# Kernel optimization log

Hardware: AMD Instinct MI355X
Metric: run time of the kernel (lower is better)

## Reference

```python
import jax, jax.numpy as jnp
import numpy as np

HEADS, HD = 8, 64

def swish(x):
    return x * jax.nn.sigmoid(x)

def layer_norm(x, eps=1e-5):
    mu = jnp.mean(x, axis=-1, keepdims=True)
    var = jnp.var(x, axis=-1, keepdims=True)
    return (x - mu) / jnp.sqrt(var + eps)

def setup_inputs() -> dict:
    key = jax.random.key(0)
    k1, k2, k3 = jax.random.split(key, 3)
    B, L, D = 2, 2048, 512
    x = jax.random.normal(k1, (B, L, D), jnp.float32)
    cnn_w = jax.random.normal(k2, (HEADS * HD * 3, D, 3), jnp.float32) * 0.02
    cnn_b = jnp.zeros((HEADS * HD * 3,), jnp.float32)
    fc_w = jax.random.normal(k3, (D, HEADS * HD), jnp.float32) * 0.02
    fc_b = jnp.zeros((D,), jnp.float32)
    return {"x": x, "cnn_w": cnn_w, "cnn_b": cnn_b, "fc_w": fc_w, "fc_b": fc_b}

def reference(x, cnn_w, cnn_b, fc_w, fc_b):
    B, L, D = x.shape
    # Conv1d(dims -> heads*hd*3, kernel=3, stride=1, pad=1) on channel-first layout
    xt = jnp.transpose(x, (0, 2, 1))  # [B, D, L]
    y = jax.lax.conv_general_dilated(
        xt, cnn_w, window_strides=(1,), padding=[(1, 1)],
        dimension_numbers=("NCH", "OIH", "NCH"),
    ) + cnn_b[None, :, None]  # [B, 3*H*HD, L]
    qkv = swish(y).reshape(B, HEADS, HD * 3, L)
    q, k, v = jnp.split(qkv, 3, axis=-2)  # each [B, H, HD, L]
    # NOTE: original scales by sqrt(length), not sqrt(hd)
    scores = jnp.einsum("bhdw,bhdm->bhwm", q, k) / jnp.sqrt(jnp.float32(L))
    att = jax.nn.softmax(scores, axis=-1)  # [B, H, L, L]
    new_v = jnp.einsum("bhwm,bhdm->bwhd", att, v).reshape(B, L, HEADS * HD)
    m = swish(new_v @ fc_w.T + fc_b)  # [B, L, D]
    return layer_norm(x * 2 + m)
```

## Files before the change

kernel.cpp:

```cpp
#include <hip/hip_runtime.h>
#include <hip/hip_bf16.h>

#define BB 2
#define LL 2048
#define DD 512
#define HH 8
#define HDM 64
#define SCALE 0.022097086912079608f
#define QSCALE 0.03187935766f

typedef __hip_bfloat16 bf16;
typedef unsigned short u16;
typedef __attribute__((ext_vector_type(8))) short short8v;
typedef __attribute__((ext_vector_type(4))) float float4v;

#define XN  2097152
#define WN  2359296
#define BN  1536
#define FWN 262144
#define FBN 512

__device__ __forceinline__ float b2f(u16 u) {
    return __uint_as_float(((unsigned int)u) << 16);
}
__device__ __forceinline__ u16 f2u(float f) {
    bf16 h = __float2bfloat16(f);
    u16 r;
    __builtin_memcpy(&r, &h, 2);
    return r;
}
__device__ __forceinline__ uint4 pack8(const float* f) {
    uint4 p;
    p.x = (unsigned)f2u(f[0]) | ((unsigned)f2u(f[1]) << 16);
    p.y = (unsigned)f2u(f[2]) | ((unsigned)f2u(f[3]) << 16);
    p.z = (unsigned)f2u(f[4]) | ((unsigned)f2u(f[5]) << 16);
    p.w = (unsigned)f2u(f[6]) | ((unsigned)f2u(f[7]) << 16);
    return p;
}

__device__ __forceinline__ void gld_lds16(const u16* g, u16* l) {
    __builtin_amdgcn_global_load_lds(
        (const __attribute__((address_space(1))) unsigned int*)g,
        (__attribute__((address_space(3))) unsigned int*)l, 16, 0, 0);
}

__device__ __forceinline__ int detect_flag(const u16* __restrict__ xraw) {
    int bad = 0;
    int lane = threadIdx.x & 63;
    for (int i = lane; i < 256; i += 64) {
        float v = b2f(xraw[i]);
        if (!(fabsf(v) < 100.f)) bad = 1;
    }
    return (__ballot(bad) != 0ull) ? 1 : 0;
}

__device__ __forceinline__ void conv8(const void* src, u16* dst, size_t i, int flag) {
    if (flag) {
        const float* s = (const float*)src;
        float f[8];
        float4 a = *(const float4*)(s + i);
        float4 b = *(const float4*)(s + i + 4);
        f[0] = a.x; f[1] = a.y; f[2] = a.z; f[3] = a.w;
        f[4] = b.x; f[5] = b.y; f[6] = b.z; f[7] = b.w;
        *(uint4*)(dst + i) = pack8(f);
    } else {
        *(uint4*)(dst + i) = *(const uint4*)((const u16*)src + i);
    }
}

__global__ __launch_bounds__(256) void prep_kernel(
    const void* __restrict__ xsrc, const void* __restrict__ wsrc,
    const void* __restrict__ bsrc, const void* __restrict__ fwsrc,
    const void* __restrict__ fbsrc,
    u16* __restrict__ xp, u16* __restrict__ wt,
    u16* __restrict__ bc, u16* __restrict__ fwc, u16* __restrict__ fbc)
{
    const int flag = detect_flag((const u16*)xsrc);
    const int bid = blockIdx.x;

    if (bid < 1024) {
        int idx = bid * 256 + threadIdx.x;
        if (idx < 256) {
            int b2  = idx >> 7;
            int r2  = (idx >> 6) & 1;
            int c82 = (idx & 63) * 8;
            size_t off = ((size_t)(b2 * 2050 + (r2 ? 2049 : 0))) * 512 + c82;
            uint4 z = {0u, 0u, 0u, 0u};
            *(uint4*)(xp + off) = z;
        }
        int b   = idx / (LL * 64);
        int rem = idx - b * (LL * 64);
        int l   = rem >> 6;
        int c8  = (rem & 63) * 8;
        size_t si = ((size_t)(b * LL + l)) * 512 + c8;
        size_t di = ((size_t)(b * 2050 + l + 1)) * 512 + c8;
        if (flag) {
            const float* s = (const float*)xsrc;
            float f[8];
            float4 a = *(const float4*)(s + si);
            float4 bq = *(const float4*)(s + si + 4);
            f[0] = a.x; f[1] = a.y; f[2] = a.z; f[3] = a.w;
            f[4] = bq.x; f[5] = bq.y; f[6] = bq.z; f[7] = bq.w;
            *(uint4*)(xp + di) = pack8(f);
        } else {
            *(uint4*)(xp + di) = *(const uint4*)((const u16*)xsrc + si);
        }
    } else if (bid < 1216) {
        __shared__ u16 wl[8 * 1536];
        const int t  = threadIdx.x;
        const int o0 = (bid - 1024) * 8;
        if (flag) {
            const float4* s4 = (const float4*)((const float*)wsrc + (size_t)o0 * 1536);
#pragma unroll
            for (int v = 0; v < 12; ++v) {
                int i4 = v * 256 + t;
                float4 q = s4[i4];
                uint2 p;
                p.x = (unsigned)f2u(q.x) | ((unsigned)f2u(q.y) << 16);
                p.y = (unsigned)f2u(q.z) | ((unsigned)f2u(q.w) << 16);
                *(uint2*)&wl[i4 * 4] = p;
            }
        } else {
            const uint4* s8 = (const uint4*)((const u16*)wsrc + (size_t)o0 * 1536);
#pragma unroll
            for (int v = 0; v < 6; ++v) {
                int i8 = v * 256 + t;
                *(uint4*)&wl[i8 * 8] = s8[i8];
            }
        }
        __syncthreads();
#pragma unroll
        for (int v = 0; v < 6; ++v) {
            int oct = v * 256 + t;
            int row = oct / 192;
            int rem = oct - row * 192;
            int k   = rem >> 6;
            int i8  = rem & 63;
            u16 tmp[8];
#pragma unroll
            for (int j = 0; j < 8; ++j) tmp[j] = wl[row * 1536 + (i8 * 8 + j) * 3 + k];
            uint4 val;
            val.x = (unsigned)tmp[0] | ((unsigned)tmp[1] << 16);
            val.y = (unsigned)tmp[2] | ((unsigned)tmp[3] << 16);
            val.z = (unsigned)tmp[4] | ((unsigned)tmp[5] << 16);
            val.w = (unsigned)tmp[6] | ((unsigned)tmp[7] << 16);
            *(uint4*)(wt + (size_t)(o0 + row) * 1536 + k * 512 + i8 * 8) = val;
        }
    } else {
        int o = (bid - 1216) * 256 + threadIdx.x;
        if (o < BN / 8) {
            conv8(bsrc, bc, (size_t)o * 8, flag);
        } else if (o < BN / 8 + FWN / 8) {
            conv8(fwsrc, fwc, (size_t)(o - BN / 8) * 8, flag);
        } else if (o < BN / 8 + FWN / 8 + FBN / 8) {
            conv8(fbsrc, fbc, (size_t)(o - BN / 8 - FWN / 8) * 8, flag);
        }
    }
}

__global__ __launch_bounds__(256) void conv_mfma_kernel(
    const u16* __restrict__ xp,
    const u16* __restrict__ wt,
    const u16* __restrict__ bias,
    u16* __restrict__ qkbuf,
    u16* __restrict__ vbuf)
{
    __shared__ u16 smem[32768];
    u16* Asb = smem;
    u16* Bsb = smem + 2 * 128 * 64;
#define OTS 140
    u16* OT  = smem;

    const int blk = blockIdx.x;
    const int rt = blk / 12;
    const int ct = blk - rt * 12;
    const int b  = rt >> 4;
    const int l0 = (rt & 15) * 128;
    const int tid  = threadIdx.x;
    const int wave = tid >> 6;
    const int lane = tid & 63;
    const int quad = lane >> 4;
    const int l16  = lane & 15;
    const int e7   = l16 & 7;
    const int wx = wave & 1;
    const int wy = wave >> 1;

    float4v acc[4][4];
#pragma unroll
    for (int mt = 0; mt < 4; ++mt)
#pragma unroll
        for (int nt = 0; nt < 4; ++nt) acc[mt][nt] = (float4v){0.f, 0.f, 0.f, 0.f};

    const int rowW = wave * 32;
    const int lrow = lane >> 3;
    const int g8   = (((lane & 7) ^ lrow)) * 8;
    auto stage = [&](int kc, int buf) {
        const int slab = kc >> 3;
        const int i0   = (kc & 7) * 64;
        const u16* ga = xp + ((size_t)(b * 2050 + l0 + rowW + slab + lrow)) * 512 + i0 + g8;
        const u16* gb = wt + ((size_t)(ct * 128 + rowW + lrow)) * 1536 + kc * 64 + g8;
        u16* la = Asb + (size_t)(buf * 128 + rowW) * 64;
        u16* lb = Bsb + (size_t)(buf * 128 + rowW) * 64;
#pragma unroll
        for (int j = 0; j < 4; ++j) {
            gld_lds16(ga + (size_t)(j * 8) * 512,  la + (j * 8) * 64);
            gld_lds16(gb + (size_t)(j * 8) * 1536, lb + (j * 8) * 64);
        }
    };

    stage(0, 0);

    for (int kc = 0; kc < 24; ++kc) {
        const int cur = kc & 1;
        __syncthreads();

        if (kc < 23) stage(kc + 1, 1 - cur);

#pragma unroll
        for (int half = 0; half < 2; ++half) {
            const int p = ((half * 4 + quad) ^ e7) * 8;
            short8v aF[4], bF[4];
#pragma unroll
            for (int mt = 0; mt < 4; ++mt)
                aF[mt] = *(const short8v*)&Asb[(size_t)(cur * 128 + wy * 64 + mt * 16 + l16) * 64 + p];
#pragma unroll
            for (int nt = 0; nt < 4; ++nt)
                bF[nt] = *(const short8v*)&Bsb[(size_t)(cur * 128 + wx * 64 + nt * 16 + l16) * 64 + p];
#pragma unroll
            for (int mt = 0; mt < 4; ++mt)
#pragma unroll
                for (int nt = 0; nt < 4; ++nt)
                    acc[mt][nt] = __builtin_amdgcn_mfma_f32_16x16x32_bf16(
                        aF[mt], bF[nt], acc[mt][nt], 0, 0, 0);
        }
    }

    __syncthreads();
    {
        const int tloc = (ct * 2 + wx) % 3;
#pragma unroll
        for (int nt = 0; nt < 4; ++nt) {
            int oc = wx * 64 + nt * 16 + l16;
            float bb = b2f(bias[ct * 128 + oc]);
#pragma unroll
            for (int mt = 0; mt < 4; ++mt)
#pragma unroll
                for (int r = 0; r < 4; ++r) {
                    int lr = wy * 64 + mt * 16 + quad * 4 + r;
                    float y = acc[mt][nt][r] + bb;
                    y = y / (1.f + __expf(-y));
                    if (tloc == 0) y *= QSCALE;
                    OT[lr * OTS + oc] = f2u(y);
                }
        }
    }
    __syncthreads();

#pragma unroll
    for (int g = 0; g < 2; ++g) {
        int a  = ct * 2 + g;
        int t  = a % 3;
        int bh = b * HH + a / 3;
        if (t != 2) {
            u16* base = qkbuf + ((size_t)((bh * 2 + t) * LL + l0)) * HDM;
#pragma unroll
            for (int it = 0; it < 4; ++it) {
                int idx = it * 256 + tid;
                int l   = idx >> 3;
                int d8  = (idx & 7) * 8;
                uint4 val = *(const uint4*)&OT[l * OTS + g * 64 + d8];
                *(uint4*)(base + (size_t)l * HDM + d8) = val;
            }
        } else {
            u16* base = vbuf + ((size_t)(bh * HDM)) * LL + l0;
#pragma unroll
            for (int it = 0; it < 4; ++it) {
                int idx = it * 256 + tid;
                int dd  = idx >> 4;
                int p   = idx & 15;
                int l8  = p * 8;
                u16 tmp[8];
#pragma unroll
                for (int j = 0; j < 8; ++j) tmp[j] = OT[(l8 + j) * OTS + g * 64 + dd];
                int a32 = p >> 2;
                int pb_ = p & 3;
                int q2  = (2 * pb_) & 3;
                int h2  = pb_ >> 1;
                int n0  = 32 * a32 + 8 * q2 + 4 * h2;
                uint2 v0, v1;
                v0.x = (unsigned)tmp[0] | ((unsigned)tmp[1] << 16);
                v0.y = (unsigned)tmp[2] | ((unsigned)tmp[3] << 16);
                v1.x = (unsigned)tmp[4] | ((unsigned)tmp[5] << 16);
                v1.y = (unsigned)tmp[6] | ((unsigned)tmp[7] << 16);
                *(uint2*)(base + (size_t)dd * LL + n0)     = v0;
                *(uint2*)(base + (size_t)dd * LL + n0 + 8) = v1;
            }
        }
    }
#undef OTS
}

__global__ __launch_bounds__(512) void attn_mfma_kernel(
    const u16* __restrict__ qk,
    const u16* __restrict__ v,
    u16* __restrict__ newv)
{
    __shared__ u16 smem[65536];
    u16 (*kts)[2][64][64] = (u16 (*)[2][64][64])smem;
    u16 (*vts)[2][64][64] = (u16 (*)[2][64][64])(smem + 32768);

    const int lb = ((blockIdx.x & 7) << 5) + (blockIdx.x >> 3);
    const int bh = lb >> 4;
    const int qc = lb & 15;
    const int b  = bh >> 3;
    const int h  = bh & 7;
    const int tid  = threadIdx.x;
    const int wave = tid >> 6;
    const int kg   = wave >> 1;
    const int qg   = wave & 1;
    const int lane = tid & 63;
    const int quad = lane >> 4;
    const int l16  = lane & 15;
    const int e7   = l16 & 7;

    const u16* qbase = qk + ((size_t)(bh * 2 + 0)) * LL * HDM;
    const u16* kbase = qk + ((size_t)(bh * 2 + 1)) * LL * HDM;
    const u16* vbase = v + (size_t)bh * HDM * LL;

    const int q0 = qc * 128 + qg * 64;

    short8v qfrag[4][2];
#pragma unroll
    for (int sg = 0; sg < 4; ++sg) {
        const u16* qr = qbase + (size_t)(q0 + sg * 16 + l16) * HDM + quad * 8;
        qfrag[sg][0] = *(const short8v*)(qr);
        qfrag[sg][1] = *(const short8v*)(qr + 32);
    }

    short8v vones;
    {
        short o1 = (l16 == 0) ? (short)0x3F80 : (short)0;
#pragma unroll
        for (int j = 0; j < 8; ++j) vones[j] = o1;
    }

    float4v oacc[4][4];
    float4v lacc[4];
#pragma unroll
    for (int sg = 0; sg < 4; ++sg) {
        lacc[sg] = (float4v){0.f, 0.f, 0.f, 0.f};
#pragma unroll
        for (int dt = 0; dt < 4; ++dt) oacc[sg][dt] = (float4v){0.f, 0.f, 0.f, 0.f};
    }

    const int rw8 = lane >> 3;
    const int sw8 = ((lane & 7) ^ rw8) * 8;
    auto stage = [&](int ic, int buf) {
        const int m0 = ic * 64;
#pragma unroll
        for (int r = 0; r < 4; ++r) {
            const int row0 = r * 16 + qg * 8;
            gld_lds16(kbase + (size_t)(m0 + row0 + rw8) * HDM + sw8,
                      &kts[kg][buf][row0][0]);
            gld_lds16(vbase + (size_t)(row0 + rw8) * LL + m0 + sw8,
                      &vts[kg][buf][row0][0]);
        }
    };

    stage(kg, 0);

    for (int i = 0; i < 8; ++i) {
        const int cur = i & 1;
        __syncthreads();

        if (i < 7) stage(4 * (i + 1) + kg, 1 - cur);

        unsigned pk[4][4][2];
#pragma unroll
        for (int mt = 0; mt < 4; ++mt) {
            short8v b0 = *(const short8v*)&kts[kg][cur][mt * 16 + l16][((quad) ^ e7) * 8];
            short8v b1 = *(const short8v*)&kts[kg][cur][mt * 16 + l16][((quad + 4) ^ e7) * 8];
#pragma unroll
            for (int sg = 0; sg < 4; ++sg) {
                float4v t = (float4v){0.f, 0.f, 0.f, 0.f};
                t = __builtin_amdgcn_mfma_f32_16x16x32_bf16(b0, qfrag[sg][0], t, 0, 0, 0);
                t = __builtin_amdgcn_mfma_f32_16x16x32_bf16(b1, qfrag[sg][1], t, 0, 0, 0);
                float p0 = __builtin_amdgcn_exp2f(t[0]);
                float p1 = __builtin_amdgcn_exp2f(t[1]);
                float p2 = __builtin_amdgcn_exp2f(t[2]);
                float p3 = __builtin_amdgcn_exp2f(t[3]);
                pk[sg][mt][0] = (unsigned)f2u(p0) | ((unsigned)f2u(p1) << 16);
                pk[sg][mt][1] = (unsigned)f2u(p2) | ((unsigned)f2u(p3) << 16);
            }
        }

#pragma unroll
        for (int mu = 0; mu < 2; ++mu) {
            short8v pb[4];
#pragma unroll
            for (int sg = 0; sg < 4; ++sg) {
                union { short8v v8; unsigned u[4]; } U;
                U.u[0] = pk[sg][2 * mu][0];
                U.u[1] = pk[sg][2 * mu][1];
                U.u[2] = pk[sg][2 * mu + 1][0];
                U.u[3] = pk[sg][2 * mu + 1][1];
                pb[sg] = U.v8;
                lacc[sg] = __builtin_amdgcn_mfma_f32_16x16x32_bf16(vones, pb[sg], lacc[sg], 0, 0, 0);
            }
#pragma unroll
            for (int dt = 0; dt < 4; ++dt) {
                short8v va = *(const short8v*)&vts[kg][cur][dt * 16 + l16][((mu * 4 + quad) ^ e7) * 8];
#pragma unroll
                for (int sg = 0; sg < 4; ++sg)
                    oacc[sg][dt] = __builtin_amdgcn_mfma_f32_16x16x32_bf16(va, pb[sg], oacc[sg][dt], 0, 0, 0);
            }
        }
    }

    float dnm[4];
#pragma unroll
    for (int sg = 0; sg < 4; ++sg) dnm[sg] = __shfl(lacc[sg][0], l16);

    __syncthreads();
    float* xch = (float*)smem;
#define XRG (2 * 68 * 64)
    if (kg > 0) {
        float* rg = xch + (kg - 1) * XRG + qg * (68 * 64);
#pragma unroll
        for (int sg = 0; sg < 4; ++sg) {
#pragma unroll
            for (int dt = 0; dt < 4; ++dt)
#pragma unroll
                for (int r = 0; r < 4; ++r)
                    rg[((sg * 16 + dt * 4 + r) << 6) + lane] = oacc[sg][dt][r];
            rg[((64 + sg) << 6) + lane] = dnm[sg];
        }
    }
    __syncthreads();
    if (kg == 0) {
        u16* ob = newv + (size_t)b * LL * 512 + h * 64;
        const float* rg = xch + qg * (68 * 64);
#pragma unroll
        for (int sg = 0; sg < 4; ++sg) {
            float dsum = dnm[sg];
#pragma unroll
            for (int p = 0; p < 3; ++p) dsum += rg[p * XRG + ((64 + sg) << 6) + lane];
            float inv = 1.f / dsum;
            const size_t orow = (size_t)(q0 + sg * 16 + l16) * 512 + quad * 4;
#pragma unroll
            for (int dt = 0; dt < 4; ++dt) {
                float o[4];
#pragma unroll
                for (int r = 0; r < 4; ++r) {
                    o[r] = oacc[sg][dt][r];
#pragma unroll
                    for (int p = 0; p < 3; ++p)
                        o[r] += rg[p * XRG + ((sg * 16 + dt * 4 + r) << 6) + lane];
                }
                unsigned lo = (unsigned)f2u(o[0] * inv) | ((unsigned)f2u(o[1] * inv) << 16);
                unsigned hi = (unsigned)f2u(o[2] * inv) | ((unsigned)f2u(o[3] * inv) << 16);
                uint2 val; val.x = lo; val.y = hi;
                *(uint2*)(ob + orow + dt * 16) = val;
            }
        }
    }
#undef XRG
}

__global__ __launch_bounds__(512) void fc_ln_mfma_kernel(
    const u16* __restrict__ newv,
    const u16* __restrict__ fcw,
    const u16* __restrict__ fcb,
    const u16* __restrict__ xp,
    const u16* __restrict__ xraw,
    void* __restrict__ out)
{
    const int flag = detect_flag(xraw);
    const int l0 = blockIdx.x * 16;
    const int tid  = threadIdx.x;
    const int wave = tid >> 6;
    const int lane = tid & 63;
    const int quad = lane >> 4;
    const int l16  = lane & 15;
    const int col0 = wave * 64;

    const int bb_ = l0 >> 11;
    const size_t xbase = ((size_t)(bb_ * 2050 + (l0 & 2047) + 1)) * 512;

    __shared__ u16 As[16][512];
    __shared__ float psum[8][16], psq[8][16];

#pragma unroll
    for (int r = 0; r < 2; ++r) {
        const int row = wave + r * 8;
        gld_lds16(newv + (size_t)(l0 + row) * 512 + ((lane ^ (row & 7)) * 8),
                  &As[row][0]);
    }
    __syncthreads();

    short8v aF[16];
#pragma unroll
    for (int kc = 0; kc < 16; ++kc)
        aF[kc] = *(const short8v*)&As[l16][(((kc * 4 + quad)) ^ (l16 & 7)) * 8];

    float4v acc[4];
#pragma unroll
    for (int nt = 0; nt < 4; ++nt) acc[nt] = (float4v){0.f, 0.f, 0.f, 0.f};

#pragma unroll
    for (int nt = 0; nt < 4; ++nt) {
        const u16* brow = fcw + (size_t)(col0 + nt * 16 + l16) * 512 + quad * 8;
#pragma unroll
        for (int kc = 0; kc < 16; ++kc) {
            short8v bF = *(const short8v*)(brow + kc * 32);
            acc[nt] = __builtin_amdgcn_mfma_f32_16x16x32_bf16(aF[kc], bF, acc[nt], 0, 0, 0);
        }
    }

    float z[4][4];
    float rs[4] = {0.f, 0.f, 0.f, 0.f}, rq[4] = {0.f, 0.f, 0.f, 0.f};
#pragma unroll
    for (int nt = 0; nt < 4; ++nt) {
        int col = col0 + nt * 16 + l16;
        float bb = b2f(fcb[col]);
#pragma unroll
        for (int r = 0; r < 4; ++r) {
            int row = quad * 4 + r;
            float y = acc[nt][r] + bb;
            float sw = y / (1.f + __expf(-y));
            float xv = b2f(xp[xbase + (size_t)row * 512 + col]);
            float zz = xv * 2.f + sw;
            z[nt][r] = zz;
            rs[r] += zz;
            rq[r] += zz * zz;
        }
    }
#pragma unroll
    for (int msk = 1; msk <= 8; msk <<= 1)
#pragma unroll
        for (int r = 0; r < 4; ++r) {
            rs[r] += __shfl_xor(rs[r], msk);
            rq[r] += __shfl_xor(rq[r], msk);
        }
    if (l16 == 0) {
#pragma unroll
        for (int r = 0; r < 4; ++r) {
            psum[wave][quad * 4 + r] = rs[r];
            psq[wave][quad * 4 + r]  = rq[r];
        }
    }
    __syncthreads();

    float mu[4], inv[4];
#pragma unroll
    for (int r = 0; r < 4; ++r) {
        int row = quad * 4 + r;
        float s = 0.f, q = 0.f;
#pragma unroll
        for (int w = 0; w < 8; ++w) { s += psum[w][row]; q += psq[w][row]; }
        float m = s * (1.f / 512.f);
        float var = q * (1.f / 512.f) - m * m;
        mu[r] = m;
        inv[r] = rsqrtf(var + 1e-5f);
    }

#pragma unroll
    for (int nt = 0; nt < 4; ++nt) {
        int col = col0 + nt * 16 + l16;
#pragma unroll
        for (int r = 0; r < 4; ++r) {
            int row = quad * 4 + r;
            float val = (z[nt][r] - mu[r]) * inv[r];
            if (flag) ((float*)out)[(size_t)(l0 + row) * 512 + col] = val;
            else      ((u16*)out)[(size_t)(l0 + row) * 512 + col] = f2u(val);
        }
    }
}

extern "C" void kernel_launch(void* const* d_in, const int* in_sizes, int n_in,
                              void* d_out, int out_size, void* d_ws, size_t ws_size,
                              hipStream_t stream) {
    (void)in_sizes; (void)n_in; (void)out_size; (void)ws_size;

    char* ws = (char*)d_ws;
    u16* xp   = (u16*)(ws + 256);
    u16* wtc  = (u16*)(ws + 4198656);
    u16* bc   = (u16*)(ws + 8917248);
    u16* fwc  = (u16*)(ws + 8920320);
    u16* fbc  = (u16*)(ws + 9444608);
    u16* qkb  = (u16*)(ws + 9445632);
    u16* vb   = (u16*)(ws + 17834240);
    u16* nvc  = (u16*)(ws + 22028544);

    prep_kernel<<<dim3(1345), dim3(256), 0, stream>>>(
        d_in[0], d_in[1], d_in[2], d_in[3], d_in[4],
        xp, wtc, bc, fwc, fbc);

    conv_mfma_kernel<<<dim3(32 * 12), dim3(256), 0, stream>>>(xp, wtc, bc, qkb, vb);
    attn_mfma_kernel<<<dim3(256), dim3(512), 0, stream>>>(qkb, vb, nvc);
    fc_ln_mfma_kernel<<<dim3(256), dim3(512), 0, stream>>>(
        nvc, fwc, fbc, xp, (const u16*)d_in[0], d_out);
}
```

Baseline: 149.4 us.

## Retile conv GEMM to 128x192 tiles with 8 waves, one head per block

The conv-as-GEMM kernel now uses 128x192 output tiles, so each block covers one head's full q/k/v channel group. It runs 8 waves (512 threads) in a 2x4 layout, with each wave computing a 64x48 subtile. The launch shrinks from 384 blocks to 256, which lines up with the CU count and removes the tail wave. The epilogue simplifies because the q/k/v split is now fixed per block. In exchange, LDS use per block goes up and per-wave accumulator reuse is slightly lower (4x3 instead of 4x4).

```diff
diff --git a/kernel.cpp b/kernel.cpp
--- a/kernel.cpp
+++ b/kernel.cpp
@@ -158,22 +158,22 @@
     }
 }
 
-__global__ __launch_bounds__(256) void conv_mfma_kernel(
+__global__ __launch_bounds__(512) void conv_mfma_kernel(
     const u16* __restrict__ xp,
     const u16* __restrict__ wt,
     const u16* __restrict__ bias,
     u16* __restrict__ qkbuf,
     u16* __restrict__ vbuf)
 {
-    __shared__ u16 smem[32768];
+    __shared__ u16 smem[40960];
     u16* Asb = smem;
-    u16* Bsb = smem + 2 * 128 * 64;
-#define OTS 140
+    u16* Bsb = smem + 16384;
+#define OTS 204
     u16* OT  = smem;
 
     const int blk = blockIdx.x;
-    const int rt = blk / 12;
-    const int ct = blk - rt * 12;
+    const int rt = blk >> 3;
+    const int ct = blk & 7;
     const int b  = rt >> 4;
     const int l0 = (rt & 15) * 128;
     const int tid  = threadIdx.x;
@@ -182,29 +182,31 @@
     const int quad = lane >> 4;
     const int l16  = lane & 15;
     const int e7   = l16 & 7;
-    const int wx = wave & 1;
-    const int wy = wave >> 1;
-
-    float4v acc[4][4];
+    const int wm = wave >> 2;
+    const int wn = wave & 3;
+
+    float4v acc[4][3];
 #pragma unroll
     for (int mt = 0; mt < 4; ++mt)
 #pragma unroll
-        for (int nt = 0; nt < 4; ++nt) acc[mt][nt] = (float4v){0.f, 0.f, 0.f, 0.f};
-
-    const int rowW = wave * 32;
+        for (int nt = 0; nt < 3; ++nt) acc[mt][nt] = (float4v){0.f, 0.f, 0.f, 0.f};
+
     const int lrow = lane >> 3;
     const int g8   = (((lane & 7) ^ lrow)) * 8;
     auto stage = [&](int kc, int buf) {
         const int slab = kc >> 3;
         const int i0   = (kc & 7) * 64;
-        const u16* ga = xp + ((size_t)(b * 2050 + l0 + rowW + slab + lrow)) * 512 + i0 + g8;
-        const u16* gb = wt + ((size_t)(ct * 128 + rowW + lrow)) * 1536 + kc * 64 + g8;
-        u16* la = Asb + (size_t)(buf * 128 + rowW) * 64;
-        u16* lb = Bsb + (size_t)(buf * 128 + rowW) * 64;
-#pragma unroll
-        for (int j = 0; j < 4; ++j) {
-            gld_lds16(ga + (size_t)(j * 8) * 512,  la + (j * 8) * 64);
-            gld_lds16(gb + (size_t)(j * 8) * 1536, lb + (j * 8) * 64);
+#pragma unroll
+        for (int j = 0; j < 2; ++j) {
+            const int r0 = wave * 16 + j * 8;
+            gld_lds16(xp + ((size_t)(b * 2050 + l0 + r0 + slab + lrow)) * 512 + i0 + g8,
+                      Asb + (size_t)(buf * 128 + r0) * 64);
+        }
+#pragma unroll
+        for (int j = 0; j < 3; ++j) {
+            const int r0 = wave * 24 + j * 8;
+            gld_lds16(wt + ((size_t)(ct * 192 + r0 + lrow)) * 1536 + kc * 64 + g8,
+                      Bsb + (size_t)(buf * 192 + r0) * 64);
         }
     };
 
@@ -219,17 +221,17 @@
 #pragma unroll
         for (int half = 0; half < 2; ++half) {
             const int p = ((half * 4 + quad) ^ e7) * 8;
-            short8v aF[4], bF[4];
+            short8v aF[4], bF[3];
 #pragma unroll
             for (int mt = 0; mt < 4; ++mt)
-                aF[mt] = *(const short8v*)&Asb[(size_t)(cur * 128 + wy * 64 + mt * 16 + l16) * 64 + p];
-#pragma unroll
-            for (int nt = 0; nt < 4; ++nt)
-                bF[nt] = *(const short8v*)&Bsb[(size_t)(cur * 128 + wx * 64 + nt * 16 + l16) * 64 + p];
+                aF[mt] = *(const short8v*)&Asb[(size_t)(cur * 128 + wm * 64 + mt * 16 + l16) * 64 + p];
+#pragma unroll
+            for (int nt = 0; nt < 3; ++nt)
+                bF[nt] = *(const short8v*)&Bsb[(size_t)(cur * 192 + wn * 48 + nt * 16 + l16) * 64 + p];
 #pragma unroll
             for (int mt = 0; mt < 4; ++mt)
 #pragma unroll
-                for (int nt = 0; nt < 4; ++nt)
+                for (int nt = 0; nt < 3; ++nt)
                     acc[mt][nt] = __builtin_amdgcn_mfma_f32_16x16x32_bf16(
                         aF[mt], bF[nt], acc[mt][nt], 0, 0, 0);
         }
@@ -237,35 +239,32 @@
 
     __syncthreads();
     {
-        const int tloc = (ct * 2 + wx) % 3;
-#pragma unroll
-        for (int nt = 0; nt < 4; ++nt) {
-            int oc = wx * 64 + nt * 16 + l16;
-            float bb = b2f(bias[ct * 128 + oc]);
+#pragma unroll
+        for (int nt = 0; nt < 3; ++nt) {
+            int oc = wn * 48 + nt * 16 + l16;
+            float bb = b2f(bias[ct * 192 + oc]);
 #pragma unroll
             for (int mt = 0; mt < 4; ++mt)
 #pragma unroll
                 for (int r = 0; r < 4; ++r) {
-                    int lr = wy * 64 + mt * 16 + quad * 4 + r;
+                    int lr = wm * 64 + mt * 16 + quad * 4 + r;
                     float y = acc[mt][nt][r] + bb;
                     y = y / (1.f + __expf(-y));
-                    if (tloc == 0) y *= QSCALE;
+                    if (oc < 64) y *= QSCALE;
                     OT[lr * OTS + oc] = f2u(y);
                 }
         }
     }
     __syncthreads();
 
-#pragma unroll
-    for (int g = 0; g < 2; ++g) {
-        int a  = ct * 2 + g;
-        int t  = a % 3;
-        int bh = b * HH + a / 3;
-        if (t != 2) {
-            u16* base = qkbuf + ((size_t)((bh * 2 + t) * LL + l0)) * HDM;
-#pragma unroll
-            for (int it = 0; it < 4; ++it) {
-                int idx = it * 256 + tid;
+    const int bh = b * HH + ct;
+#pragma unroll
+    for (int g = 0; g < 3; ++g) {
+        if (g != 2) {
+            u16* base = qkbuf + ((size_t)((bh * 2 + g) * LL + l0)) * HDM;
+#pragma unroll
+            for (int it = 0; it < 2; ++it) {
+                int idx = it * 512 + tid;
                 int l   = idx >> 3;
                 int d8  = (idx & 7) * 8;
                 uint4 val = *(const uint4*)&OT[l * OTS + g * 64 + d8];
@@ -274,8 +273,8 @@
         } else {
             u16* base = vbuf + ((size_t)(bh * HDM)) * LL + l0;
 #pragma unroll
-            for (int it = 0; it < 4; ++it) {
-                int idx = it * 256 + tid;
+            for (int it = 0; it < 2; ++it) {
+                int idx = it * 512 + tid;
                 int dd  = idx >> 4;
                 int p   = idx & 15;
                 int l8  = p * 8;
@@ -596,7 +595,7 @@
         d_in[0], d_in[1], d_in[2], d_in[3], d_in[4],
         xp, wtc, bc, fwc, fbc);
 
-    conv_mfma_kernel<<<dim3(32 * 12), dim3(256), 0, stream>>>(xp, wtc, bc, qkb, vb);
+    conv_mfma_kernel<<<dim3(256), dim3(512), 0, stream>>>(xp, wtc, bc, qkb, vb);
     attn_mfma_kernel<<<dim3(256), dim3(512), 0, stream>>>(qkb, vb, nvc);
     fc_ln_mfma_kernel<<<dim3(256), dim3(512), 0, stream>>>(
         nvc, fwc, fbc, xp, (const u16*)d_in[0], d_out);
```

Result: faster. 145.8 us (-2.4%).
